# Kernel optimization log

Hardware: AMD Instinct MI355X
Metric: run time of the kernel (lower is better)

## Reference

```python
import jax, jax.numpy as jnp
import numpy as np

BITS = 4
SIGNED_MIN, SIGNED_MAX = -(2 ** (BITS - 1)), 2 ** (BITS - 1) - 1      # int4: [-8, 7]
UNSIGNED_MIN, UNSIGNED_MAX = 0, 2 ** BITS - 1                          # uint4: [0, 15]
INT32_MIN, INT32_MAX = -(2.0 ** 31), 2.0 ** 31 - 1


def fake_quant(x, scale, qmin, qmax):
    """Brevitas-style fake quantization with straight-through rounding."""
    q = jnp.clip(jnp.round(x / scale), qmin, qmax) * scale
    # STE: identity gradient through round/clip
    return x + jax.lax.stop_gradient(q - x)


def weight_scale(W):
    # Brevitas default weight quantizer: per-tensor scale from max-abs stats
    return jax.lax.stop_gradient(jnp.max(jnp.abs(W))) / SIGNED_MAX


def setup_inputs() -> dict:
    key = jax.random.key(0)
    ks = jax.random.split(key, 5)
    B, S, D, F = 4, 2048, 2048, 8192
    return {
        "x": jax.random.normal(ks[0], (B, S, D), dtype=jnp.float32),
        "W1": jax.random.normal(ks[1], (F, D), dtype=jnp.float32) * 0.02,
        "b1": jax.random.normal(ks[2], (F,), dtype=jnp.float32) * 0.02,
        "W2": jax.random.normal(ks[3], (D, F), dtype=jnp.float32) * 0.02,
        "b2": jax.random.normal(ks[4], (D,), dtype=jnp.float32) * 0.02,
        "s_act1": jnp.full((1,), 0.1, dtype=jnp.float32),
        "s_act2": jnp.full((1,), 0.1, dtype=jnp.float32),
    }


def reference(x, W1, b1, W2, b2, s_act1, s_act2):
    s1 = s_act1[0]
    s2 = s_act2[0]

    # quantizer_1: signed int4 QuantIdentity on input
    x_q = fake_quant(x, s1, SIGNED_MIN, SIGNED_MAX)

    # w_1: int4 weight QuantLinear with Int32Bias (bias scale = in_scale * w_scale)
    sw1 = weight_scale(W1)
    W1_q = fake_quant(W1, sw1, SIGNED_MIN, SIGNED_MAX)
    b1_q = fake_quant(b1, s1 * sw1, INT32_MIN, INT32_MAX)
    h = jnp.einsum("bsd,fd->bsf", x_q, W1_q) + b1_q  # [B, S, d_ff]

    # quantizer_2: QuantReLU -> unsigned int4 fake-quant of relu(h)
    h_q = fake_quant(jax.nn.relu(h), s2, UNSIGNED_MIN, UNSIGNED_MAX)
    # dropout: identity in eval mode

    # w_2: int4 weight QuantLinear, input scale = s2
    sw2 = weight_scale(W2)
    W2_q = fake_quant(W2, sw2, SIGNED_MIN, SIGNED_MAX)
    b2_q = fake_quant(b2, s2 * sw2, INT32_MIN, INT32_MAX)
    out = jnp.einsum("bsf,df->bsd", h_q, W2_q) + b2_q  # [B, S, d_model]
    return out
```

## Files before the change

### kernel.cpp

```cpp
#include <hip/hip_runtime.h>

typedef int int32x4 __attribute__((ext_vector_type(4)));

__global__ void maxabs_kernel(const float* __restrict__ x, int n4,
                              unsigned* __restrict__ out) {
    float m = 0.f;
    int i = blockIdx.x * blockDim.x + threadIdx.x;
    int stride = gridDim.x * blockDim.x;
    const float4* x4 = (const float4*)x;
    for (int j = i; j < n4; j += stride) {
        float4 v = x4[j];
        m = fmaxf(m, fmaxf(fmaxf(fabsf(v.x), fabsf(v.y)),
                           fmaxf(fabsf(v.z), fabsf(v.w))));
    }
#pragma unroll
    for (int off = 32; off; off >>= 1)
        m = fmaxf(m, __shfl_down(m, off, 64));
    __shared__ float wm[4];
    int ln = threadIdx.x & 63, wv = threadIdx.x >> 6;
    if (ln == 0) wm[wv] = m;
    __syncthreads();
    if (threadIdx.x == 0) {
        float bm = fmaxf(fmaxf(wm[0], wm[1]), fmaxf(wm[2], wm[3]));
        atomicMax(out, __float_as_uint(bm));
    }
}

__global__ void quant_blocked_kernel(const float* __restrict__ src, int n4,
                                     int K, int kshift,
                                     const float* __restrict__ sptr, float sdiv,
                                     float lo, float hi, int* __restrict__ out) {
    float s = sptr[0] / sdiv;
    int i0 = blockIdx.x * blockDim.x + threadIdx.x;
    int stride = gridDim.x * blockDim.x;
    for (int o = i0; o < n4; o += stride) {
        int blk = o >> 11;
        int i = o & 2047;
        int v = i >> 5;
        int sc = (i >> 2) & 7;
        int w = i & 3;
        int vc = sc ^ (v & 7);
        int row = (v << 1) | (vc >> 2);
        int chunk = vc & 3;
        int rowblk = blk >> kshift;
        int kblk = blk & ((1 << kshift) - 1);
        long srcoff = (long)(rowblk * 128 + row) * K + (kblk << 6) + (chunk << 4) + (w << 2);
        float4 f = *(const float4*)(src + srcoff);
        int a = (int)fminf(fmaxf(rintf(f.x / s), lo), hi);
        int b = (int)fminf(fmaxf(rintf(f.y / s), lo), hi);
        int c = (int)fminf(fmaxf(rintf(f.z / s), lo), hi);
        int d = (int)fminf(fmaxf(rintf(f.w / s), lo), hi);
        out[o] = (a & 255) | ((b & 255) << 8) | ((c & 255) << 16) | ((d & 255) << 24);
    }
}

template <bool FIRST>
__global__ __launch_bounds__(256, 4)
void gemm_i8_kernel(const char* __restrict__ A, const char* __restrict__ B,
                    int N, int nkt,
                    const float* __restrict__ sa_ptr,
                    const float* __restrict__ wmax_ptr,
                    const float* __restrict__ bias,
                    const float* __restrict__ s2_ptr,
                    char* __restrict__ out8, float* __restrict__ outf) {
    __shared__ __align__(16) char lA[128 * 64];
    __shared__ __align__(16) char lB[128 * 64];

    const int tid = threadIdx.x;
    const int wv = tid >> 6, ln = tid & 63;
    const int lnlo = ln & 15, lnhi = ln >> 4;
    const int wr = wv >> 1, wc = wv & 1;

    int32x4 acc[4][4] = {};

    const char* pa = A + ((size_t)blockIdx.y * nkt << 13);
    const char* pb = B + ((size_t)blockIdx.x * nkt << 13);

    for (int kt = 0; kt < nkt; ++kt) {
#pragma unroll
        for (int r = 0; r < 2; ++r) {
            int off = (r * 256 + tid) * 16;
            int lbase = (r * 256 + wv * 64) * 16;
            __builtin_amdgcn_global_load_lds(
                (const __attribute__((address_space(1))) void*)(pa + off),
                (__attribute__((address_space(3))) void*)(lA + lbase), 16, 0, 0);
            __builtin_amdgcn_global_load_lds(
                (const __attribute__((address_space(1))) void*)(pb + off),
                (__attribute__((address_space(3))) void*)(lB + lbase), 16, 0, 0);
        }
        pa += 8192;
        pb += 8192;
        __syncthreads();

        int32x4 af[4], bf[4];
#pragma unroll
        for (int mf = 0; mf < 4; ++mf) {
            int row = wr * 64 + mf * 16 + lnlo;
            int v = row >> 1;
            int vc = ((row & 1) << 2) | lnhi;
            af[mf] = *(const int32x4*)(lA + v * 128 + ((vc ^ (v & 7)) << 4));
        }
#pragma unroll
        for (int nf = 0; nf < 4; ++nf) {
            int col = wc * 64 + nf * 16 + lnlo;
            int v = col >> 1;
            int vc = ((col & 1) << 2) | lnhi;
            bf[nf] = *(const int32x4*)(lB + v * 128 + ((vc ^ (v & 7)) << 4));
        }

#pragma unroll
        for (int mf = 0; mf < 4; ++mf)
#pragma unroll
            for (int nf = 0; nf < 4; ++nf)
                acc[mf][nf] = __builtin_amdgcn_mfma_i32_16x16x64_i8(
                    af[mf], bf[nf], acc[mf][nf], 0, 0, 0);
        __syncthreads();
    }

    float sa = sa_ptr[0];
    float sw = wmax_ptr[0] / 7.0f;
    float sab = sa * sw;
    float s2v = FIRST ? s2_ptr[0] : 0.f;

#pragma unroll
    for (int nf = 0; nf < 4; ++nf) {
        int lc = wc * 64 + nf * 16 + lnlo;
        long col = (long)blockIdx.x * 128 + lc;
        float bq = rintf(bias[col] / sab) * sab;
#pragma unroll
        for (int mf = 0; mf < 4; ++mf) {
            int lr0 = wr * 64 + mf * 16 + (lnhi << 2);
#pragma unroll
            for (int i = 0; i < 4; ++i) {
                int lr = lr0 + i;
                float h = sab * (float)acc[mf][nf][i] + bq;
                if constexpr (FIRST) {
                    h = fmaxf(h, 0.f);
                    float qv = fminf(fmaxf(rintf(h / s2v), 0.f), 15.f);
                    int kblk = (blockIdx.x << 1) | (lc >> 6);
                    int l6 = lc & 63;
                    int v = lr >> 1;
                    int vc = ((lr & 1) << 2) | (l6 >> 4);
                    size_t blkoff =
                        ((size_t)blockIdx.y * (gridDim.x << 1) + kblk) << 13;
                    out8[blkoff + v * 128 + ((vc ^ (v & 7)) << 4) + (lc & 15)] =
                        (char)(int)qv;
                } else {
                    outf[((long)blockIdx.y * 128 + lr) * N + col] = h;
                }
            }
        }
    }
}

extern "C" void kernel_launch(void* const* d_in, const int* in_sizes, int n_in,
                              void* d_out, int out_size, void* d_ws, size_t ws_size,
                              hipStream_t stream) {
    const float* x  = (const float*)d_in[0];
    const float* W1 = (const float*)d_in[1];
    const float* b1 = (const float*)d_in[2];
    const float* W2 = (const float*)d_in[3];
    const float* b2 = (const float*)d_in[4];
    const float* s1 = (const float*)d_in[5];
    const float* s2 = (const float*)d_in[6];

    const int M = 8192, D = 2048, F = 8192;

    char* ws = (char*)d_ws;
    unsigned* mx1 = (unsigned*)ws;
    unsigned* mx2 = (unsigned*)(ws + 4);
    char* xq  = ws + 256;
    char* w1q = xq + (size_t)M * D;
    char* w2q = w1q + (size_t)F * D;
    char* hq  = w2q + (size_t)D * F;

    hipMemsetAsync(d_ws, 0, 8, stream);

    maxabs_kernel<<<2048, 256, 0, stream>>>(W1, (F * D) >> 2, mx1);
    maxabs_kernel<<<2048, 256, 0, stream>>>(W2, (D * F) >> 2, mx2);

    quant_blocked_kernel<<<2048, 256, 0, stream>>>(
        x,  (M * D) >> 2, D, 5, s1, 1.f, -8.f, 7.f, (int*)xq);
    quant_blocked_kernel<<<2048, 256, 0, stream>>>(
        W1, (F * D) >> 2, D, 5, (const float*)mx1, 7.f, -8.f, 7.f, (int*)w1q);
    quant_blocked_kernel<<<2048, 256, 0, stream>>>(
        W2, (D * F) >> 2, F, 7, (const float*)mx2, 7.f, -8.f, 7.f, (int*)w2q);

    gemm_i8_kernel<true><<<dim3(F / 128, M / 128), 256, 0, stream>>>(
        xq, w1q, F, D / 64, s1, (const float*)mx1, b1, s2, hq, nullptr);

    gemm_i8_kernel<false><<<dim3(D / 128, M / 128), 256, 0, stream>>>(
        hq, w2q, D, F / 64, s2, (const float*)mx2, b2, nullptr, nullptr,
        (float*)d_out);
}
```

Baseline: 375.4 us.

## Double-buffer LDS tiles in int8 GEMM and merge max-abs kernels

The GEMM now uses two LDS buffers per operand. It issues the global-to-LDS loads for the next K tile before computing the current one, waiting on vmcnt instead of a full sync, and raises wave priority around the MFMA block. The goal is to hide global load latency behind matrix math. The two per-weight max-abs reductions are also merged into one launch using blockIdx.y to pick the weight, which removes a kernel launch. Doubling LDS per block to 32KB may lower occupancy, and the manual vmcnt counts depend on exactly four loads per stage.

```diff
diff --git a/kernel.cpp b/kernel.cpp
--- a/kernel.cpp
+++ b/kernel.cpp
@@ -2,12 +2,13 @@
 
 typedef int int32x4 __attribute__((ext_vector_type(4)));
 
-__global__ void maxabs_kernel(const float* __restrict__ x, int n4,
-                              unsigned* __restrict__ out) {
+__global__ void maxabs2_kernel(const float* __restrict__ w1,
+                               const float* __restrict__ w2, int n4,
+                               unsigned* __restrict__ out) {
+    const float4* x4 = (const float4*)(blockIdx.y ? w2 : w1);
     float m = 0.f;
     int i = blockIdx.x * blockDim.x + threadIdx.x;
     int stride = gridDim.x * blockDim.x;
-    const float4* x4 = (const float4*)x;
     for (int j = i; j < n4; j += stride) {
         float4 v = x4[j];
         m = fmaxf(m, fmaxf(fmaxf(fabsf(v.x), fabsf(v.y)),
@@ -22,7 +23,7 @@
     __syncthreads();
     if (threadIdx.x == 0) {
         float bm = fmaxf(fmaxf(wm[0], wm[1]), fmaxf(wm[2], wm[3]));
-        atomicMax(out, __float_as_uint(bm));
+        atomicMax(out + blockIdx.y, __float_as_uint(bm));
     }
 }
 
@@ -63,8 +64,8 @@
                     const float* __restrict__ bias,
                     const float* __restrict__ s2_ptr,
                     char* __restrict__ out8, float* __restrict__ outf) {
-    __shared__ __align__(16) char lA[128 * 64];
-    __shared__ __align__(16) char lB[128 * 64];
+    __shared__ __align__(16) char lA[2][128 * 64];
+    __shared__ __align__(16) char lB[2][128 * 64];
 
     const int tid = threadIdx.x;
     const int wv = tid >> 6, ln = tid & 63;
@@ -73,48 +74,65 @@
 
     int32x4 acc[4][4] = {};
 
-    const char* pa = A + ((size_t)blockIdx.y * nkt << 13);
-    const char* pb = B + ((size_t)blockIdx.x * nkt << 13);
-
-    for (int kt = 0; kt < nkt; ++kt) {
+    const char* pa0 = A + ((size_t)blockIdx.y * nkt << 13);
+    const char* pb0 = B + ((size_t)blockIdx.x * nkt << 13);
+
+    auto stage = [&](int t) {
+        const int buf = t & 1;
+        const char* pa = pa0 + ((size_t)t << 13);
+        const char* pb = pb0 + ((size_t)t << 13);
 #pragma unroll
         for (int r = 0; r < 2; ++r) {
             int off = (r * 256 + tid) * 16;
             int lbase = (r * 256 + wv * 64) * 16;
             __builtin_amdgcn_global_load_lds(
                 (const __attribute__((address_space(1))) void*)(pa + off),
-                (__attribute__((address_space(3))) void*)(lA + lbase), 16, 0, 0);
+                (__attribute__((address_space(3))) void*)(lA[buf] + lbase), 16, 0, 0);
             __builtin_amdgcn_global_load_lds(
                 (const __attribute__((address_space(1))) void*)(pb + off),
-                (__attribute__((address_space(3))) void*)(lB + lbase), 16, 0, 0);
-        }
-        pa += 8192;
-        pb += 8192;
-        __syncthreads();
-
+                (__attribute__((address_space(3))) void*)(lB[buf] + lbase), 16, 0, 0);
+        }
+    };
+
+    stage(0);
+
+    for (int t = 0; t < nkt; ++t) {
+        if (t + 1 < nkt) {
+            stage(t + 1);
+            asm volatile("s_waitcnt vmcnt(4)" ::: "memory");
+        } else {
+            asm volatile("s_waitcnt vmcnt(0)" ::: "memory");
+        }
+        __builtin_amdgcn_s_barrier();
+        __builtin_amdgcn_sched_barrier(0);
+
+        const char* la = lA[t & 1];
+        const char* lb = lB[t & 1];
         int32x4 af[4], bf[4];
 #pragma unroll
         for (int mf = 0; mf < 4; ++mf) {
             int row = wr * 64 + mf * 16 + lnlo;
             int v = row >> 1;
             int vc = ((row & 1) << 2) | lnhi;
-            af[mf] = *(const int32x4*)(lA + v * 128 + ((vc ^ (v & 7)) << 4));
+            af[mf] = *(const int32x4*)(la + v * 128 + ((vc ^ (v & 7)) << 4));
         }
 #pragma unroll
         for (int nf = 0; nf < 4; ++nf) {
             int col = wc * 64 + nf * 16 + lnlo;
             int v = col >> 1;
             int vc = ((col & 1) << 2) | lnhi;
-            bf[nf] = *(const int32x4*)(lB + v * 128 + ((vc ^ (v & 7)) << 4));
-        }
-
+            bf[nf] = *(const int32x4*)(lb + v * 128 + ((vc ^ (v & 7)) << 4));
+        }
+
+        __builtin_amdgcn_s_setprio(1);
 #pragma unroll
         for (int mf = 0; mf < 4; ++mf)
 #pragma unroll
             for (int nf = 0; nf < 4; ++nf)
                 acc[mf][nf] = __builtin_amdgcn_mfma_i32_16x16x64_i8(
                     af[mf], bf[nf], acc[mf][nf], 0, 0, 0);
-        __syncthreads();
+        __builtin_amdgcn_s_setprio(0);
+        __builtin_amdgcn_s_barrier();
     }
 
     float sa = sa_ptr[0];
@@ -167,8 +185,7 @@
     const int M = 8192, D = 2048, F = 8192;
 
     char* ws = (char*)d_ws;
-    unsigned* mx1 = (unsigned*)ws;
-    unsigned* mx2 = (unsigned*)(ws + 4);
+    unsigned* mx = (unsigned*)ws;
     char* xq  = ws + 256;
     char* w1q = xq + (size_t)M * D;
     char* w2q = w1q + (size_t)F * D;
@@ -176,20 +193,19 @@
 
     hipMemsetAsync(d_ws, 0, 8, stream);
 
-    maxabs_kernel<<<2048, 256, 0, stream>>>(W1, (F * D) >> 2, mx1);
-    maxabs_kernel<<<2048, 256, 0, stream>>>(W2, (D * F) >> 2, mx2);
+    maxabs2_kernel<<<dim3(2048, 2), 256, 0, stream>>>(W1, W2, (F * D) >> 2, mx);
 
     quant_blocked_kernel<<<2048, 256, 0, stream>>>(
         x,  (M * D) >> 2, D, 5, s1, 1.f, -8.f, 7.f, (int*)xq);
     quant_blocked_kernel<<<2048, 256, 0, stream>>>(
-        W1, (F * D) >> 2, D, 5, (const float*)mx1, 7.f, -8.f, 7.f, (int*)w1q);
+        W1, (F * D) >> 2, D, 5, (const float*)mx, 7.f, -8.f, 7.f, (int*)w1q);
     quant_blocked_kernel<<<2048, 256, 0, stream>>>(
-        W2, (D * F) >> 2, F, 7, (const float*)mx2, 7.f, -8.f, 7.f, (int*)w2q);
+        W2, (D * F) >> 2, F, 7, (const float*)(mx + 1), 7.f, -8.f, 7.f, (int*)w2q);
 
     gemm_i8_kernel<true><<<dim3(F / 128, M / 128), 256, 0, stream>>>(
-        xq, w1q, F, D / 64, s1, (const float*)mx1, b1, s2, hq, nullptr);
+        xq, w1q, F, D / 64, s1, (const float*)mx, b1, s2, hq, nullptr);
 
     gemm_i8_kernel<false><<<dim3(D / 128, M / 128), 256, 0, stream>>>(
-        hq, w2q, D, F / 64, s2, (const float*)mx2, b2, nullptr, nullptr,
+        hq, w2q, D, F / 64, s2, (const float*)(mx + 1), b2, nullptr, nullptr,
         (float*)d_out);
 }
```

Result: no change. 372.9 us (-0.7%).
